# Optimization experiments

Measured on AMD Instinct MI355X. Metric: run time of the kernel, lower is better.

The kernel has to match this reference:

```python
import jax, jax.numpy as jnp
import numpy as np


def pixel_coordinates(h, w):
    # (h, w, 2) grid of (x, y) in [-1, 1]
    y = jnp.linspace(-1.0, 1.0, h)
    x = jnp.linspace(-1.0, 1.0, w)
    yy, xx = jnp.meshgrid(y, x, indexing='ij')
    return jnp.stack([xx, yy], axis=-1)


def base_grid(h_in, w_in):
    y = jnp.linspace(-1.0 + 1.0 / h_in, 1.0 - 1.0 / h_in, h_in)
    x = jnp.linspace(-1.0 + 1.0 / w_in, 1.0 - 1.0 / w_in, w_in)
    yy, xx = jnp.meshgrid(y, x, indexing='ij')
    return jnp.stack([xx, yy], axis=-1)  # [h_in, w_in, 2]


def setup_inputs() -> dict:
    key = jax.random.key(0)
    params = jax.random.normal(key, (2, 9, 32, 32), dtype=jnp.float32)
    return {"params": params, "h_out": 128, "w_out": 128}


def reference(params, h_out, w_out):
    B, _, h_in, w_in = params.shape
    N = h_in * w_in
    p = jnp.transpose(params, (0, 2, 3, 1))  # [B, h_in, w_in, 9]

    # positions (mu): base grid + tanh(offset) * (2/h_in)
    mu = base_grid(h_in, w_in)[None] + jnp.tanh(p[..., 0:2]) * (2.0 / h_in)
    mu = mu.reshape(B, N, 2)

    # covariance via Cholesky-like factor L = [[exp(a), 0], [b, exp(c)]]
    v1x = jnp.exp(p[..., 2])
    v2x = p[..., 3]
    v2y = jnp.exp(p[..., 4])
    zero = jnp.zeros_like(v1x)
    L = jnp.stack([jnp.stack([v1x, zero], axis=-1),
                   jnp.stack([v2x, v2y], axis=-1)], axis=-2)  # [B,h,w,2,2]
    cov = L @ jnp.swapaxes(L, -1, -2)
    cov = cov.reshape(B, N, 2, 2) + jnp.eye(2, dtype=params.dtype) * 1e-5
    Sigma_inv = jnp.linalg.inv(cov)  # [B, N, 2, 2]

    colors = jax.nn.sigmoid(p[..., 5:8]).reshape(B, N, 3)
    opacities = jax.nn.sigmoid(p[..., 8]).reshape(B, N)

    coords = pixel_coordinates(h_out, w_out)  # [H, W, 2]
    dx = coords[None, None] - mu[:, :, None, None, :]  # [B, N, H, W, 2]
    exponent = -0.5 * jnp.einsum('bnhwi,bnij,bnhwj->bnhw', dx, Sigma_inv, dx)
    exponent = jnp.clip(exponent, -20.0, 20.0)
    kernel = jnp.exp(exponent)  # [B, N, H, W]

    weights = opacities[:, :, None, None] * kernel
    weights_sum = jnp.sum(weights, axis=1, keepdims=True) + 1e-8
    norm_w = weights / weights_sum  # [B, N, H, W]
    image = jnp.einsum('bnhw,bnc->bchw', norm_w, colors)  # [B, 3, H, W]
    return image
```

## Files before the change

kernel.cpp:

```cpp
#include <hip/hip_runtime.h>


#define NB   2
#define NG   1024
#define HOUT 128
#define WOUT 128
#define PSTRIDE 20
#define NCHUNK 16

typedef float v2f __attribute__((ext_vector_type(2)));

__device__ __forceinline__ float fast_exp(float x) {
    return __builtin_amdgcn_exp2f(x * 1.4426950408889634f);
}
__device__ __forceinline__ float fast_sigmoid(float x) {
    float e = __builtin_amdgcn_exp2f(-x * 1.4426950408889634f);
    return __builtin_amdgcn_rcpf(1.0f + e);
}
__device__ __forceinline__ float fast_tanh(float x) {
    float e = __builtin_amdgcn_exp2f(-x * 2.8853900817779268f);
    return fmaf(2.0f, __builtin_amdgcn_rcpf(1.0f + e), -1.0f);
}

__global__ __launch_bounds__(1024, 8) void gauss_fused(const float* __restrict__ params,
                                                       float* __restrict__ out) {
    __shared__ __align__(16) float gtab[(NG / 2) * PSTRIDE];
    __shared__ float4 sred[1024];

    const int tx  = threadIdx.x;
    const int ty  = threadIdx.y;
    const int tid = ty * 64 + tx;
    const int blk = blockIdx.x;
    const int b   = blk >> 8;

    {
        const int n = tid;
        const int gh = n >> 5;
        const int gw = n & 31;

        const float* P = params + b * 9 * NG + n;
        float p0 = P[0 * NG];
        float p1 = P[1 * NG];
        float p2 = P[2 * NG];
        float p3 = P[3 * NG];
        float p4 = P[4 * NG];
        float p5 = P[5 * NG];
        float p6 = P[6 * NG];
        float p7 = P[7 * NG];
        float p8 = P[8 * NG];

        float mux = -0.96875f + (float)gw * 0.0625f + fast_tanh(p0) * 0.0625f;
        float muy = -0.96875f + (float)gh * 0.0625f + fast_tanh(p1) * 0.0625f;

        float ea  = fast_exp(p2);
        float ec  = fast_exp(p4);
        float c00 = ea * ea + 1e-5f;
        float c01 = p3 * ea;
        float c11 = p3 * p3 + ec * ec + 1e-5f;
        float det = c00 * c11 - c01 * c01;
        float id  = 1.0f / det;
        float Sa  =  c11 * id;
        float Sb  = -c01 * id;
        float Sc  =  c00 * id;

        const float s = -0.72134752044448169f;
        float A  = s * Sa;
        float B2 = 2.0f * s * Sb;
        float C  = s * Sc;

        float cr = fast_sigmoid(p5);
        float cg = fast_sigmoid(p6);
        float cb = fast_sigmoid(p7);
        float op = fast_sigmoid(p8);

        float* o = gtab + (n >> 1) * PSTRIDE + (n & 1);
        o[0]  = mux;  o[2]  = muy;  o[4]  = A;       o[6]  = B2;
        o[8]  = C;    o[10] = op;   o[12] = op * cr; o[14] = op * cg;
        o[16] = op * cb;
    }
    __syncthreads();

    const int pix = ((blk & 255) << 6) + tx;
    const int h = pix >> 7;
    const int w = pix & 127;
    const float px = -1.0f + (float)w * (2.0f / 127.0f);
    const float py = -1.0f + (float)h * (2.0f / 127.0f);
    const v2f px2 = {px, px};
    const v2f py2 = {py, py};

    const v2f* __restrict__ gp =
        (const v2f*)(gtab + ty * (NG / 2 / NCHUNK) * PSTRIDE);

    v2f wsum2 = {0.0f, 0.0f}, ar2 = {0.0f, 0.0f};
    v2f ag2   = {0.0f, 0.0f}, ab2 = {0.0f, 0.0f};

    #pragma unroll 2
    for (int j = 0; j < NG / 2 / NCHUNK; ++j) {
        const v2f* __restrict__ r = gp + j * (PSTRIDE / 2);
        v2f mux2 = r[0], muy2 = r[1];
        v2f A2   = r[2], B22  = r[3], C2 = r[4];
        v2f op2  = r[5], ocr2 = r[6], ocg2 = r[7], ocb2 = r[8];

        v2f dx = px2 - mux2;
        v2f dy = py2 - muy2;
        v2f m  = A2 * dx;
        m      = __builtin_elementwise_fma(B22, dy, m);
        v2f t  = C2 * dy;
        v2f e2 = __builtin_elementwise_fma(t, dy, m * dx);
        e2 = __builtin_elementwise_max(e2, (v2f){-28.853900817779268f,
                                                 -28.853900817779268f});
        v2f k2 = {__builtin_amdgcn_exp2f(e2.x), __builtin_amdgcn_exp2f(e2.y)};

        wsum2 = __builtin_elementwise_fma(op2,  k2, wsum2);
        ar2   = __builtin_elementwise_fma(ocr2, k2, ar2);
        ag2   = __builtin_elementwise_fma(ocg2, k2, ag2);
        ab2   = __builtin_elementwise_fma(ocb2, k2, ab2);
    }

    sred[tid] = make_float4(wsum2.x + wsum2.y, ar2.x + ar2.y,
                            ag2.x + ag2.y,     ab2.x + ab2.y);
    __syncthreads();

    if (ty == 0) {
        float4 a = sred[tx];
        #pragma unroll
        for (int k2i = 1; k2i < NCHUNK; ++k2i) {
            float4 t = sred[k2i * 64 + tx];
            a.x += t.x; a.y += t.y; a.z += t.z; a.w += t.w;
        }
        float inv = 1.0f / (a.x + 1e-8f);
        float* ob = out + b * 3 * (HOUT * WOUT) + pix;
        ob[0]               = a.y * inv;
        ob[HOUT * WOUT]     = a.z * inv;
        ob[2 * HOUT * WOUT] = a.w * inv;
    }
}

extern "C" void kernel_launch(void* const* d_in, const int* in_sizes, int n_in,
                              void* d_out, int out_size, void* d_ws, size_t ws_size,
                              hipStream_t stream) {
    const float* params = (const float*)d_in[0];
    float* out = (float*)d_out;
    (void)d_ws; (void)ws_size;

    hipLaunchKernelGGL(gauss_fused, dim3(NB * (HOUT * WOUT) / 64), dim3(64, 16),
                       0, stream, params, out);
}
```

Before: 68.01 us.

## Hold gaussian records in registers and reduce per pixel with DPP wave sums

Each lane now keeps 16 gaussians (8 paired records) in registers instead of staging all 1024 in LDS. Each wave loops over 16 pixels and uses a DPP cross-lane reduction to sum contributions over the gaussian dimension. This removes the LDS table, the LDS reads in the inner loop, and the shared-memory reduction with its barriers. In exchange it adds six DPP reduction steps per accumulator per pixel, a serial store from one lane, and heavy register pressure from the 144-float record array.

```diff
diff --git a/kernel.cpp b/kernel.cpp
--- a/kernel.cpp
+++ b/kernel.cpp
@@ -5,8 +5,7 @@
 #define NG   1024
 #define HOUT 128
 #define WOUT 128
-#define PSTRIDE 20
-#define NCHUNK 16
+#define NPW  16
 
 typedef float v2f __attribute__((ext_vector_type(2)));
 
@@ -22,117 +21,120 @@
     return fmaf(2.0f, __builtin_amdgcn_rcpf(1.0f + e), -1.0f);
 }
 
-__global__ __launch_bounds__(1024, 8) void gauss_fused(const float* __restrict__ params,
-                                                       float* __restrict__ out) {
-    __shared__ __align__(16) float gtab[(NG / 2) * PSTRIDE];
-    __shared__ float4 sred[1024];
+template<int CTRL, int RM>
+__device__ __forceinline__ float dpp_add(float v) {
+    int s = __builtin_amdgcn_update_dpp(0, __float_as_int(v), CTRL, RM, 0xF, true);
+    return v + __int_as_float(s);
+}
+__device__ __forceinline__ float wave_sum(float v) {
+    v = dpp_add<0x111, 0xF>(v);
+    v = dpp_add<0x112, 0xF>(v);
+    v = dpp_add<0x114, 0xF>(v);
+    v = dpp_add<0x118, 0xF>(v);
+    v = dpp_add<0x142, 0xA>(v);
+    v = dpp_add<0x143, 0xC>(v);
+    return v;
+}
 
-    const int tx  = threadIdx.x;
-    const int ty  = threadIdx.y;
-    const int tid = ty * 64 + tx;
-    const int blk = blockIdx.x;
-    const int b   = blk >> 8;
+struct Coefs { float A, B2, C; };
+__device__ __forceinline__ Coefs cov_coefs(float p2, float p3, float p4) {
+    float ea  = fast_exp(p2);
+    float ec  = fast_exp(p4);
+    float c00 = ea * ea + 1e-5f;
+    float c01 = p3 * ea;
+    float c11 = p3 * p3 + ec * ec + 1e-5f;
+    float det = c00 * c11 - c01 * c01;
+    float id  = 1.0f / det;
+    const float s = -0.72134752044448169f;
+    Coefs r;
+    r.A  = s * c11 * id;
+    r.B2 = -2.0f * s * c01 * id;
+    r.C  = s * c00 * id;
+    return r;
+}
 
-    {
-        const int n = tid;
-        const int gh = n >> 5;
-        const int gw = n & 31;
+__global__ __launch_bounds__(256, 2) void gauss_all(const float* __restrict__ params,
+                                                    float* __restrict__ out) {
+    const int tid  = threadIdx.x;
+    const int lane = tid & 63;
+    const int wv   = tid >> 6;
+    const int blk  = blockIdx.x;
+    const int b    = blk >> 8;
+    const int pix0 = (((blk & 255) << 2) + wv) * NPW;
 
-        const float* P = params + b * 9 * NG + n;
-        float p0 = P[0 * NG];
-        float p1 = P[1 * NG];
-        float p2 = P[2 * NG];
-        float p3 = P[3 * NG];
-        float p4 = P[4 * NG];
-        float p5 = P[5 * NG];
-        float p6 = P[6 * NG];
-        float p7 = P[7 * NG];
-        float p8 = P[8 * NG];
+    v2f rec[8][9];
+    const float* P = params + b * 9 * NG;
+    #pragma unroll
+    for (int k = 0; k < 8; ++k) {
+        const int n0 = 2 * lane + 128 * k;
+        v2f p[9];
+        #pragma unroll
+        for (int f = 0; f < 9; ++f)
+            p[f] = *(const v2f*)(P + f * NG + n0);
 
-        float mux = -0.96875f + (float)gw * 0.0625f + fast_tanh(p0) * 0.0625f;
-        float muy = -0.96875f + (float)gh * 0.0625f + fast_tanh(p1) * 0.0625f;
+        const float gw = (float)(n0 & 31);
+        const float gh = (float)(n0 >> 5);
+        v2f mux2, muy2, A2, B22, C2;
+        mux2.x = -0.96875f + gw * 0.0625f + fast_tanh(p[0].x) * 0.0625f;
+        mux2.y = -0.96875f + (gw + 1.0f) * 0.0625f + fast_tanh(p[0].y) * 0.0625f;
+        muy2.x = -0.96875f + gh * 0.0625f + fast_tanh(p[1].x) * 0.0625f;
+        muy2.y = -0.96875f + gh * 0.0625f + fast_tanh(p[1].y) * 0.0625f;
+        Coefs cx = cov_coefs(p[2].x, p[3].x, p[4].x);
+        Coefs cy = cov_coefs(p[2].y, p[3].y, p[4].y);
+        A2.x = cx.A; B22.x = cx.B2; C2.x = cx.C;
+        A2.y = cy.A; B22.y = cy.B2; C2.y = cy.C;
+        v2f op2, ocr2, ocg2, ocb2;
+        op2.x  = fast_sigmoid(p[8].x);         op2.y  = fast_sigmoid(p[8].y);
+        ocr2.x = op2.x * fast_sigmoid(p[5].x); ocr2.y = op2.y * fast_sigmoid(p[5].y);
+        ocg2.x = op2.x * fast_sigmoid(p[6].x); ocg2.y = op2.y * fast_sigmoid(p[6].y);
+        ocb2.x = op2.x * fast_sigmoid(p[7].x); ocb2.y = op2.y * fast_sigmoid(p[7].y);
 
-        float ea  = fast_exp(p2);
-        float ec  = fast_exp(p4);
-        float c00 = ea * ea + 1e-5f;
-        float c01 = p3 * ea;
-        float c11 = p3 * p3 + ec * ec + 1e-5f;
-        float det = c00 * c11 - c01 * c01;
-        float id  = 1.0f / det;
-        float Sa  =  c11 * id;
-        float Sb  = -c01 * id;
-        float Sc  =  c00 * id;
+        rec[k][0] = mux2; rec[k][1] = muy2; rec[k][2] = A2;
+        rec[k][3] = B22;  rec[k][4] = C2;   rec[k][5] = op2;
+        rec[k][6] = ocr2; rec[k][7] = ocg2; rec[k][8] = ocb2;
+    }
 
-        const float s = -0.72134752044448169f;
-        float A  = s * Sa;
-        float B2 = 2.0f * s * Sb;
-        float C  = s * Sc;
-
-        float cr = fast_sigmoid(p5);
-        float cg = fast_sigmoid(p6);
-        float cb = fast_sigmoid(p7);
-        float op = fast_sigmoid(p8);
-
-        float* o = gtab + (n >> 1) * PSTRIDE + (n & 1);
-        o[0]  = mux;  o[2]  = muy;  o[4]  = A;       o[6]  = B2;
-        o[8]  = C;    o[10] = op;   o[12] = op * cr; o[14] = op * cg;
-        o[16] = op * cb;
-    }
-    __syncthreads();
-
-    const int pix = ((blk & 255) << 6) + tx;
-    const int h = pix >> 7;
-    const int w = pix & 127;
-    const float px = -1.0f + (float)w * (2.0f / 127.0f);
-    const float py = -1.0f + (float)h * (2.0f / 127.0f);
-    const v2f px2 = {px, px};
+    const int w0 = pix0 & 127;
+    const int h0 = pix0 >> 7;
+    const float py = -1.0f + (float)h0 * (2.0f / 127.0f);
     const v2f py2 = {py, py};
-
-    const v2f* __restrict__ gp =
-        (const v2f*)(gtab + ty * (NG / 2 / NCHUNK) * PSTRIDE);
-
-    v2f wsum2 = {0.0f, 0.0f}, ar2 = {0.0f, 0.0f};
-    v2f ag2   = {0.0f, 0.0f}, ab2 = {0.0f, 0.0f};
+    float* ob = out + b * 3 * (HOUT * WOUT) + pix0;
 
     #pragma unroll 2
-    for (int j = 0; j < NG / 2 / NCHUNK; ++j) {
-        const v2f* __restrict__ r = gp + j * (PSTRIDE / 2);
-        v2f mux2 = r[0], muy2 = r[1];
-        v2f A2   = r[2], B22  = r[3], C2 = r[4];
-        v2f op2  = r[5], ocr2 = r[6], ocg2 = r[7], ocb2 = r[8];
+    for (int i = 0; i < NPW; ++i) {
+        const float px = -1.0f + (float)(w0 + i) * (2.0f / 127.0f);
+        const v2f px2 = {px, px};
+        v2f wsum2 = {0.0f, 0.0f}, ar2 = {0.0f, 0.0f};
+        v2f ag2   = {0.0f, 0.0f}, ab2 = {0.0f, 0.0f};
 
-        v2f dx = px2 - mux2;
-        v2f dy = py2 - muy2;
-        v2f m  = A2 * dx;
-        m      = __builtin_elementwise_fma(B22, dy, m);
-        v2f t  = C2 * dy;
-        v2f e2 = __builtin_elementwise_fma(t, dy, m * dx);
-        e2 = __builtin_elementwise_max(e2, (v2f){-28.853900817779268f,
-                                                 -28.853900817779268f});
-        v2f k2 = {__builtin_amdgcn_exp2f(e2.x), __builtin_amdgcn_exp2f(e2.y)};
+        #pragma unroll
+        for (int k = 0; k < 8; ++k) {
+            v2f dx = px2 - rec[k][0];
+            v2f dy = py2 - rec[k][1];
+            v2f m  = rec[k][2] * dx;
+            m      = __builtin_elementwise_fma(rec[k][3], dy, m);
+            v2f t  = rec[k][4] * dy;
+            v2f e2 = __builtin_elementwise_fma(t, dy, m * dx);
+            e2 = __builtin_elementwise_max(e2, (v2f){-28.853900817779268f,
+                                                     -28.853900817779268f});
+            v2f k2 = {__builtin_amdgcn_exp2f(e2.x), __builtin_amdgcn_exp2f(e2.y)};
+            wsum2 = __builtin_elementwise_fma(rec[k][5], k2, wsum2);
+            ar2   = __builtin_elementwise_fma(rec[k][6], k2, ar2);
+            ag2   = __builtin_elementwise_fma(rec[k][7], k2, ag2);
+            ab2   = __builtin_elementwise_fma(rec[k][8], k2, ab2);
+        }
 
-        wsum2 = __builtin_elementwise_fma(op2,  k2, wsum2);
-        ar2   = __builtin_elementwise_fma(ocr2, k2, ar2);
-        ag2   = __builtin_elementwise_fma(ocg2, k2, ag2);
-        ab2   = __builtin_elementwise_fma(ocb2, k2, ab2);
-    }
+        float ws = wave_sum(wsum2.x + wsum2.y);
+        float rr = wave_sum(ar2.x + ar2.y);
+        float gg = wave_sum(ag2.x + ag2.y);
+        float bb = wave_sum(ab2.x + ab2.y);
 
-    sred[tid] = make_float4(wsum2.x + wsum2.y, ar2.x + ar2.y,
-                            ag2.x + ag2.y,     ab2.x + ab2.y);
-    __syncthreads();
-
-    if (ty == 0) {
-        float4 a = sred[tx];
-        #pragma unroll
-        for (int k2i = 1; k2i < NCHUNK; ++k2i) {
-            float4 t = sred[k2i * 64 + tx];
-            a.x += t.x; a.y += t.y; a.z += t.z; a.w += t.w;
+        if (lane == 63) {
+            float inv = 1.0f / (ws + 1e-8f);
+            ob[i]                   = rr * inv;
+            ob[i + HOUT * WOUT]     = gg * inv;
+            ob[i + 2 * HOUT * WOUT] = bb * inv;
         }
-        float inv = 1.0f / (a.x + 1e-8f);
-        float* ob = out + b * 3 * (HOUT * WOUT) + pix;
-        ob[0]               = a.y * inv;
-        ob[HOUT * WOUT]     = a.z * inv;
-        ob[2 * HOUT * WOUT] = a.w * inv;
     }
 }
 
@@ -143,6 +145,5 @@
     float* out = (float*)d_out;
     (void)d_ws; (void)ws_size;
 
-    hipLaunchKernelGGL(gauss_fused, dim3(NB * (HOUT * WOUT) / 64), dim3(64, 16),
-                       0, stream, params, out);
+    hipLaunchKernelGGL(gauss_all, dim3(512), dim3(256), 0, stream, params, out);
 }
```

After: 72.81 us. 7.1% more time.

## Process two pixels per thread sharing row terms and halve block count

Applied to the files above, without the earlier changes.

Each block now covers a full 128-pixel output row, and each thread evaluates two pixels that share the same y coordinate. The per-Gaussian LDS loads and the dy-dependent terms (B*dy, C*dy*dy) are reused for both pixels, and the per-block Gaussian table setup is paid half as often because there are half as many blocks. The cost is more registers per thread, and the launch-bounds min-blocks hint is dropped. Fewer blocks (256 instead of 512) also lowers available parallelism across CUs.

```diff
diff --git a/kernel.cpp b/kernel.cpp
--- a/kernel.cpp
+++ b/kernel.cpp
@@ -22,16 +22,18 @@
     return fmaf(2.0f, __builtin_amdgcn_rcpf(1.0f + e), -1.0f);
 }
 
-__global__ __launch_bounds__(1024, 8) void gauss_fused(const float* __restrict__ params,
-                                                       float* __restrict__ out) {
+__global__ __launch_bounds__(1024) void gauss_fused(const float* __restrict__ params,
+                                                    float* __restrict__ out) {
     __shared__ __align__(16) float gtab[(NG / 2) * PSTRIDE];
-    __shared__ float4 sred[1024];
+    __shared__ float4 sred[NCHUNK][128];
 
     const int tx  = threadIdx.x;
     const int ty  = threadIdx.y;
     const int tid = ty * 64 + tx;
     const int blk = blockIdx.x;
-    const int b   = blk >> 8;
+    const int b   = blk >> 7;
+    const int row = blk & 127;
+    const int pixb = row << 7;
 
     {
         const int n = tid;
@@ -80,56 +82,67 @@
     }
     __syncthreads();
 
-    const int pix = ((blk & 255) << 6) + tx;
-    const int h = pix >> 7;
-    const int w = pix & 127;
-    const float px = -1.0f + (float)w * (2.0f / 127.0f);
-    const float py = -1.0f + (float)h * (2.0f / 127.0f);
-    const v2f px2 = {px, px};
-    const v2f py2 = {py, py};
+    const float py  = -1.0f + (float)row * (2.0f / 127.0f);
+    const float pxA = -1.0f + (float)tx * (2.0f / 127.0f);
+    const float pxB = -1.0f + (float)(tx + 64) * (2.0f / 127.0f);
+    const v2f py2  = {py, py};
+    const v2f pxA2 = {pxA, pxA};
+    const v2f pxB2 = {pxB, pxB};
 
     const v2f* __restrict__ gp =
         (const v2f*)(gtab + ty * (NG / 2 / NCHUNK) * PSTRIDE);
 
-    v2f wsum2 = {0.0f, 0.0f}, ar2 = {0.0f, 0.0f};
-    v2f ag2   = {0.0f, 0.0f}, ab2 = {0.0f, 0.0f};
+    v2f wsA = {0,0}, arA = {0,0}, agA = {0,0}, abA = {0,0};
+    v2f wsB = {0,0}, arB = {0,0}, agB = {0,0}, abB = {0,0};
 
-    #pragma unroll 2
+    #pragma unroll 4
     for (int j = 0; j < NG / 2 / NCHUNK; ++j) {
         const v2f* __restrict__ r = gp + j * (PSTRIDE / 2);
         v2f mux2 = r[0], muy2 = r[1];
         v2f A2   = r[2], B22  = r[3], C2 = r[4];
         v2f op2  = r[5], ocr2 = r[6], ocg2 = r[7], ocb2 = r[8];
 
-        v2f dx = px2 - mux2;
-        v2f dy = py2 - muy2;
-        v2f m  = A2 * dx;
-        m      = __builtin_elementwise_fma(B22, dy, m);
-        v2f t  = C2 * dy;
-        v2f e2 = __builtin_elementwise_fma(t, dy, m * dx);
-        e2 = __builtin_elementwise_max(e2, (v2f){-28.853900817779268f,
-                                                 -28.853900817779268f});
-        v2f k2 = {__builtin_amdgcn_exp2f(e2.x), __builtin_amdgcn_exp2f(e2.y)};
+        v2f dy   = py2 - muy2;
+        v2f bdy  = B22 * dy;
+        v2f cdy2 = (C2 * dy) * dy;
+        const v2f clampv = {-28.853900817779268f, -28.853900817779268f};
 
-        wsum2 = __builtin_elementwise_fma(op2,  k2, wsum2);
-        ar2   = __builtin_elementwise_fma(ocr2, k2, ar2);
-        ag2   = __builtin_elementwise_fma(ocg2, k2, ag2);
-        ab2   = __builtin_elementwise_fma(ocb2, k2, ab2);
+        v2f dxA = pxA2 - mux2;
+        v2f eA  = __builtin_elementwise_fma(
+                      dxA, __builtin_elementwise_fma(A2, dxA, bdy), cdy2);
+        eA = __builtin_elementwise_max(eA, clampv);
+        v2f kA = {__builtin_amdgcn_exp2f(eA.x), __builtin_amdgcn_exp2f(eA.y)};
+        wsA = __builtin_elementwise_fma(op2,  kA, wsA);
+        arA = __builtin_elementwise_fma(ocr2, kA, arA);
+        agA = __builtin_elementwise_fma(ocg2, kA, agA);
+        abA = __builtin_elementwise_fma(ocb2, kA, abA);
+
+        v2f dxB = pxB2 - mux2;
+        v2f eB  = __builtin_elementwise_fma(
+                      dxB, __builtin_elementwise_fma(A2, dxB, bdy), cdy2);
+        eB = __builtin_elementwise_max(eB, clampv);
+        v2f kB = {__builtin_amdgcn_exp2f(eB.x), __builtin_amdgcn_exp2f(eB.y)};
+        wsB = __builtin_elementwise_fma(op2,  kB, wsB);
+        arB = __builtin_elementwise_fma(ocr2, kB, arB);
+        agB = __builtin_elementwise_fma(ocg2, kB, agB);
+        abB = __builtin_elementwise_fma(ocb2, kB, abB);
     }
 
-    sred[tid] = make_float4(wsum2.x + wsum2.y, ar2.x + ar2.y,
-                            ag2.x + ag2.y,     ab2.x + ab2.y);
+    sred[ty][tx]      = make_float4(wsA.x + wsA.y, arA.x + arA.y,
+                                    agA.x + agA.y, abA.x + abA.y);
+    sred[ty][tx + 64] = make_float4(wsB.x + wsB.y, arB.x + arB.y,
+                                    agB.x + agB.y, abB.x + abB.y);
     __syncthreads();
 
-    if (ty == 0) {
-        float4 a = sred[tx];
+    if (tid < 128) {
+        float4 a = sred[0][tid];
         #pragma unroll
-        for (int k2i = 1; k2i < NCHUNK; ++k2i) {
-            float4 t = sred[k2i * 64 + tx];
+        for (int c = 1; c < NCHUNK; ++c) {
+            float4 t = sred[c][tid];
             a.x += t.x; a.y += t.y; a.z += t.z; a.w += t.w;
         }
         float inv = 1.0f / (a.x + 1e-8f);
-        float* ob = out + b * 3 * (HOUT * WOUT) + pix;
+        float* ob = out + b * 3 * (HOUT * WOUT) + pixb + tid;
         ob[0]               = a.y * inv;
         ob[HOUT * WOUT]     = a.z * inv;
         ob[2 * HOUT * WOUT] = a.w * inv;
@@ -143,6 +156,6 @@
     float* out = (float*)d_out;
     (void)d_ws; (void)ws_size;
 
-    hipLaunchKernelGGL(gauss_fused, dim3(NB * (HOUT * WOUT) / 64), dim3(64, 16),
-                       0, stream, params, out);
+    hipLaunchKernelGGL(gauss_fused, dim3(NB * 128), dim3(64, NCHUNK), 0, stream,
+                       params, out);
 }
```

Measured after the change: 66.15 us. 2.7% less time.
